# Kernel tuning notes

Measured on AMD Instinct MI355X. Metric: run time of the kernel, lower is better.

The kernel has to match this reference:

```python
import jax, jax.numpy as jnp
import numpy as np

B, T, F = 128, 64, 2048
N, H, C = 1024, 1024, 22  # neurons, hidden_size, num_classes


def setup_inputs() -> dict:
    key = jax.random.key(0)
    ks = jax.random.split(key, 9)
    def w(k, shape, fan_in):
        return jax.random.normal(k, shape, dtype=jnp.float32) / np.sqrt(fan_in)
    return {
        "x": jax.random.normal(ks[0], (B, T, F), dtype=jnp.float32),
        "W1": w(ks[1], (N, F), F),
        "b1": jnp.zeros((N,), jnp.float32),
        "W_ih": w(ks[2], (4 * H, N), N),
        "b_ih": jnp.zeros((4 * H,), jnp.float32),
        "W_hh": w(ks[3], (4 * H, H), H),
        "b_hh": jnp.zeros((4 * H,), jnp.float32),
        "Wc": w(ks[4], (C, H), H),
        "bc": jnp.zeros((C,), jnp.float32),
    }


def reference(x, W1, b1, W_ih, b_ih, W_hh, b_hh, Wc, bc):
    b, t, _ = x.shape
    h0 = jnp.zeros((b, H), x.dtype)
    c0 = jnp.zeros((b, H), x.dtype)
    # Precompute the input-side projections for every step (batched GEMMs):
    z = jax.nn.relu(jnp.einsum("btf,nf->btn", x, W1) + b1)        # [B,T,N]
    xg = jnp.einsum("btn,gn->btg", z, W_ih) + b_ih                 # [B,T,4H]

    def step(carry, xg_t):
        h, c = carry
        gates = xg_t + h @ W_hh.T + b_hh                           # [B,4H]
        i, f, g, o = jnp.split(gates, 4, axis=-1)                  # torch LSTMCell gate order
        c = jax.nn.sigmoid(f) * c + jax.nn.sigmoid(i) * jnp.tanh(g)
        h = jax.nn.sigmoid(o) * jnp.tanh(c)
        return (h, c), h

    _, hs = jax.lax.scan(step, (h0, c0), jnp.swapaxes(xg, 0, 1))    # hs: [T,B,H]
    scores = jnp.einsum("tbh,ch->tbc", hs, Wc) + bc                # [T,B,C]
    scores = jnp.swapaxes(scores, 0, 1).reshape(-1, Wc.shape[0])    # [B*T, C]
    return scores
```

## Files before the change

### kernel.cpp

```cpp
#include <hip/hip_runtime.h>
#include <hip/hip_bf16.h>

typedef short bf16x8 __attribute__((ext_vector_type(8)));
typedef float f32x4 __attribute__((ext_vector_type(4)));

#define B_ 128
#define T_ 64
#define F_ 2048
#define N_ 1024
#define H_ 1024
#define C_ 22

__device__ __forceinline__ ushort f2bf(float f) {
    union { float f; unsigned u; } v; v.f = f;
    unsigned u = v.u;
    unsigned r = (u + 0x7FFFu + ((u >> 16) & 1u)) >> 16;
    return (ushort)r;
}
__device__ __forceinline__ float bf2f(ushort h) {
    union { unsigned u; float f; } v; v.u = ((unsigned)h) << 16;
    return v.f;
}

__global__ __launch_bounds__(256) void cvt_f32_bf16(const float* __restrict__ in,
                                                    ushort* __restrict__ out, int n4) {
    int i = blockIdx.x * blockDim.x + threadIdx.x;
    if (i < n4) {
        float4 v = ((const float4*)in)[i];
        ushort4 o;
        o.x = f2bf(v.x); o.y = f2bf(v.y); o.z = f2bf(v.z); o.w = f2bf(v.w);
        ((ushort4*)out)[i] = o;
    }
}

__global__ __launch_bounds__(256) void cvt_wc(const float* __restrict__ Wc,
                                              ushort* __restrict__ Wcb) {
    int i = blockIdx.x * 256 + threadIdx.x;
    int row = i >> 10;
    Wcb[i] = (row < C_) ? f2bf(Wc[i]) : (ushort)0;
}

__device__ __forceinline__ void gload16(const void* g, void* l) {
    __builtin_amdgcn_global_load_lds(
        (const __attribute__((address_space(1))) unsigned int*)g,
        (__attribute__((address_space(3))) unsigned int*)l, 16, 0, 0);
}

template<int K, bool RELU>
__global__ __launch_bounds__(256) void gemm_bt(const ushort* __restrict__ A,
                                               const ushort* __restrict__ Bm,
                                               const float* __restrict__ bias1,
                                               const float* __restrict__ bias2,
                                               ushort* __restrict__ C,
                                               int Nt, int Nn) {
    __shared__ ushort sA[128 * 32];
    __shared__ ushort sB[128 * 32];
    const int tid = threadIdx.x;
    const int lane = tid & 63, wv = tid >> 6;
    const int tm = blockIdx.x / Nt, tn = blockIdx.x % Nt;
    const int wm = wv >> 1, wn = wv & 1;

    const ushort* gA = A + (size_t)(tm * 128 + (tid >> 2)) * K + (tid & 3) * 8;
    const ushort* gB = Bm + (size_t)(tn * 128 + (tid >> 2)) * K + (tid & 3) * 8;
    char* lAb = (char*)sA + wv * 1024;
    char* lBb = (char*)sB + wv * 1024;

    f32x4 acc[4][4] = {};

    for (int kt = 0; kt < K / 32; kt++) {
        const ushort* a0 = gA + kt * 32;
        const ushort* b0 = gB + kt * 32;
        gload16(a0, lAb);
        gload16(a0 + 64 * K, lAb + 4096);
        gload16(b0, lBb);
        gload16(b0 + 64 * K, lBb + 4096);
        __syncthreads();

        bf16x8 af[4], bfv[4];
#pragma unroll
        for (int i = 0; i < 4; i++)
            af[i] = *(const bf16x8*)&sA[(wm * 64 + i * 16 + (lane & 15)) * 32 + (lane >> 4) * 8];
#pragma unroll
        for (int j = 0; j < 4; j++)
            bfv[j] = *(const bf16x8*)&sB[(wn * 64 + j * 16 + (lane & 15)) * 32 + (lane >> 4) * 8];
#pragma unroll
        for (int i = 0; i < 4; i++)
#pragma unroll
            for (int j = 0; j < 4; j++)
                acc[i][j] = __builtin_amdgcn_mfma_f32_16x16x32_bf16(af[i], bfv[j], acc[i][j], 0, 0, 0);
        __syncthreads();
    }

#pragma unroll
    for (int j = 0; j < 4; j++) {
        int n = tn * 128 + wn * 64 + j * 16 + (lane & 15);
        float bias = bias1[n] + (bias2 ? bias2[n] : 0.f);
#pragma unroll
        for (int i = 0; i < 4; i++) {
            int mbase = tm * 128 + wm * 64 + i * 16 + (lane >> 4) * 4;
#pragma unroll
            for (int r = 0; r < 4; r++) {
                float v = acc[i][j][r] + bias;
                if (RELU) v = v > 0.f ? v : 0.f;
                C[(size_t)(mbase + r) * Nn + n] = f2bf(v);
            }
        }
    }
}

__global__ __launch_bounds__(256, 1) void lstm_persist(ushort* __restrict__ hs,
                                                       const ushort* __restrict__ xg,
                                                       const ushort* __restrict__ Whh,
                                                       unsigned* __restrict__ flags) {
    const int tid = threadIdx.x;
    const int lane = tid & 63;
    const int wv = tid >> 6;
    const int blk = (int)blockIdx.x;
    const int batch0 = (blk >> 6) * 32;
    const int hid0 = (blk & 63) * 16;
    const int gb = blk & ~63;

    bf16x8 breg[32];
    {
        const ushort* br = Whh + (size_t)(wv * H_ + hid0 + (lane & 15)) * H_ + ((lane >> 4) * 8);
#pragma unroll
        for (int ks = 0; ks < 32; ks++) breg[ks] = *(const bf16x8*)(br + ks * 32);
#pragma unroll
        for (int ks = 0; ks < 32; ks++) asm volatile("" : "+v"(breg[ks]));
    }

    __shared__ float lg[4][32][16];

    const int grow = tid >> 3;
    const int gjp = (tid & 7) * 2;
    float c0 = 0.f, c1 = 0.f;

    const int b = batch0 + grow;
    const int jj = hid0 + gjp;
    const ushort* xrow = xg + ((size_t)(b * T_) << 12) + jj;

    for (int t = 0; t < T_; t++) {
        const ushort* xr = xrow + ((size_t)t << 12);
        uint xi = *(const uint*)(xr);
        uint xf = *(const uint*)(xr + 1024);
        uint xgv = *(const uint*)(xr + 2048);
        uint xo = *(const uint*)(xr + 3072);

        const ushort* ar = hs + (size_t)t * (B_ * H_)
                         + (size_t)(batch0 + (lane & 15)) * H_ + ((lane >> 4) * 8);
        f32x4 acc0 = {}, acc1 = {};
#pragma unroll
        for (int ks = 0; ks < 32; ks++) {
            bf16x8 a0 = *(const bf16x8*)(ar + ks * 32);
            bf16x8 a1 = *(const bf16x8*)(ar + 16 * H_ + ks * 32);
            acc0 = __builtin_amdgcn_mfma_f32_16x16x32_bf16(a0, breg[ks], acc0, 0, 0, 0);
            acc1 = __builtin_amdgcn_mfma_f32_16x16x32_bf16(a1, breg[ks], acc1, 0, 0, 0);
        }
#pragma unroll
        for (int r = 0; r < 4; r++) {
            lg[wv][(lane >> 4) * 4 + r][lane & 15] = acc0[r];
            lg[wv][16 + (lane >> 4) * 4 + r][lane & 15] = acc1[r];
        }
        __syncthreads();

        {
            float pi0 = bf2f((ushort)(xi & 0xffff)) + lg[0][grow][gjp];
            float pi1 = bf2f((ushort)(xi >> 16)) + lg[0][grow][gjp + 1];
            float pf0 = bf2f((ushort)(xf & 0xffff)) + lg[1][grow][gjp];
            float pf1 = bf2f((ushort)(xf >> 16)) + lg[1][grow][gjp + 1];
            float pg0 = bf2f((ushort)(xgv & 0xffff)) + lg[2][grow][gjp];
            float pg1 = bf2f((ushort)(xgv >> 16)) + lg[2][grow][gjp + 1];
            float po0 = bf2f((ushort)(xo & 0xffff)) + lg[3][grow][gjp];
            float po1 = bf2f((ushort)(xo >> 16)) + lg[3][grow][gjp + 1];
            float si0 = 1.f / (1.f + expf(-pi0)), si1 = 1.f / (1.f + expf(-pi1));
            float sf0 = 1.f / (1.f + expf(-pf0)), sf1 = 1.f / (1.f + expf(-pf1));
            float tg0 = tanhf(pg0), tg1 = tanhf(pg1);
            float so0 = 1.f / (1.f + expf(-po0)), so1 = 1.f / (1.f + expf(-po1));
            c0 = sf0 * c0 + si0 * tg0;
            c1 = sf1 * c1 + si1 * tg1;
            uint hp = (uint)f2bf(so0 * tanhf(c0)) | ((uint)f2bf(so1 * tanhf(c1)) << 16);
            unsigned* hp32 = (unsigned*)(hs + (size_t)(t + 1) * (B_ * H_) + (size_t)b * H_ + jj);
            __hip_atomic_store(hp32, hp, __ATOMIC_RELAXED, __HIP_MEMORY_SCOPE_AGENT);
        }
        __syncthreads();

        if (t < T_ - 1) {
            if (tid == 0)
                __hip_atomic_store(&flags[blk * 16], (unsigned)(t + 1),
                                   __ATOMIC_RELAXED, __HIP_MEMORY_SCOPE_AGENT);
            if (wv == 0) {
                asm volatile("s_waitcnt vmcnt(0)" ::: "memory");
                for (;;) {
                    unsigned f = __hip_atomic_load(&flags[(gb + lane) * 16],
                                                   __ATOMIC_RELAXED, __HIP_MEMORY_SCOPE_AGENT);
                    if (__ballot(f < (unsigned)(t + 1)) == 0ull) break;
                    __builtin_amdgcn_s_sleep(1);
                }
            }
            __syncthreads();
        }
    }
}

__global__ __launch_bounds__(256) void scores_mfma(const ushort* __restrict__ hs,
                                                   const ushort* __restrict__ Wcb,
                                                   const float* __restrict__ bc,
                                                   float* __restrict__ out) {
    const int tid = threadIdx.x, lane = tid & 63, w = tid >> 6;
    const int r0 = blockIdx.x * 64 + w * 16;
    const int rr = r0 + (lane & 15);
    const int b = rr >> 6, t = rr & 63;
    const ushort* arow = hs + (size_t)(t + 1) * (B_ * H_) + (size_t)b * H_ + ((lane >> 4) * 8);
    const ushort* brow0 = Wcb + (size_t)(lane & 15) * H_ + ((lane >> 4) * 8);
    const ushort* brow1 = brow0 + 16 * H_;

    f32x4 acc0 = {}, acc1 = {};
#pragma unroll
    for (int ks = 0; ks < 32; ks++) {
        bf16x8 a  = *(const bf16x8*)(arow + ks * 32);
        bf16x8 p0 = *(const bf16x8*)(brow0 + ks * 32);
        bf16x8 p1 = *(const bf16x8*)(brow1 + ks * 32);
        acc0 = __builtin_amdgcn_mfma_f32_16x16x32_bf16(a, p0, acc0, 0, 0, 0);
        acc1 = __builtin_amdgcn_mfma_f32_16x16x32_bf16(a, p1, acc1, 0, 0, 0);
    }
#pragma unroll
    for (int nf = 0; nf < 2; nf++) {
        int c = nf * 16 + (lane & 15);
        if (c < C_) {
            float bias = bc[c];
            f32x4 acc = nf ? acc1 : acc0;
#pragma unroll
            for (int r = 0; r < 4; r++) {
                int row = r0 + (lane >> 4) * 4 + r;
                out[(size_t)row * C_ + c] = acc[r] + bias;
            }
        }
    }
}

extern "C" void kernel_launch(void* const* d_in, const int* in_sizes, int n_in,
                              void* d_out, int out_size, void* d_ws, size_t ws_size,
                              hipStream_t stream) {
    const float* x = (const float*)d_in[0];
    const float* W1 = (const float*)d_in[1];
    const float* b1 = (const float*)d_in[2];
    const float* W_ih = (const float*)d_in[3];
    const float* b_ih = (const float*)d_in[4];
    const float* W_hh = (const float*)d_in[5];
    const float* b_hh = (const float*)d_in[6];
    const float* Wc = (const float*)d_in[7];
    const float* bc = (const float*)d_in[8];
    float* out = (float*)d_out;

    char* ws = (char*)d_ws;
    ushort* Xb   = (ushort*)(ws);
    ushort* W1b  = (ushort*)(ws + 33554432);
    ushort* Wihb = (ushort*)(ws + 37748736);
    ushort* Whhb = (ushort*)(ws + 46137344);
    ushort* z    = (ushort*)(ws + 54525952);
    ushort* xg   = (ushort*)(ws + 71303168);
    ushort* hs   = (ushort*)(ws + 138412032);
    ushort* Wcb  = (ushort*)(ws + 155451392);
    unsigned* flags = (unsigned*)(ws + 155516928);

    hipMemsetAsync(hs, 0, (size_t)B_ * H_ * sizeof(ushort), stream);
    hipMemsetAsync(flags, 0, 16384, stream);

    cvt_f32_bf16<<<16384, 256, 0, stream>>>(x, Xb, 4194304);
    cvt_f32_bf16<<<2048, 256, 0, stream>>>(W1, W1b, 524288);
    cvt_f32_bf16<<<4096, 256, 0, stream>>>(W_ih, Wihb, 1048576);
    cvt_f32_bf16<<<4096, 256, 0, stream>>>(W_hh, Whhb, 1048576);
    cvt_wc<<<128, 256, 0, stream>>>(Wc, Wcb);

    gemm_bt<2048, true><<<512, 256, 0, stream>>>(Xb, W1b, b1, nullptr, z, 8, 1024);
    gemm_bt<1024, false><<<2048, 256, 0, stream>>>(z, Wihb, b_ih, b_hh, xg, 32, 4096);

    lstm_persist<<<256, 256, 0, stream>>>(hs, xg, Whhb, flags);

    scores_mfma<<<128, 256, 0, stream>>>(hs, Wcb, bc, out);
}
```

Measured before the change: 782.4 us.

## Repartition persistent LSTM into 16-batch x 32-hidden tiles with 8 waves

```diff
diff --git a/kernel.cpp b/kernel.cpp
--- a/kernel.cpp
+++ b/kernel.cpp
@@ -108,79 +108,75 @@
     }
 }
 
-__global__ __launch_bounds__(256, 1) void lstm_persist(ushort* __restrict__ hs,
+__global__ __launch_bounds__(512, 2) void lstm_persist(ushort* __restrict__ hs,
                                                        const ushort* __restrict__ xg,
                                                        const ushort* __restrict__ Whh,
                                                        unsigned* __restrict__ flags) {
     const int tid = threadIdx.x;
     const int lane = tid & 63;
     const int wv = tid >> 6;
+    const int g = wv >> 1;
+    const int ch = wv & 1;
     const int blk = (int)blockIdx.x;
-    const int batch0 = (blk >> 6) * 32;
-    const int hid0 = (blk & 63) * 16;
-    const int gb = blk & ~63;
+    const int bt = blk & 7;
+    const int hb = blk >> 3;
+    const int batch0 = bt * 16;
+    const int hid0 = hb * 32;
 
     bf16x8 breg[32];
     {
-        const ushort* br = Whh + (size_t)(wv * H_ + hid0 + (lane & 15)) * H_ + ((lane >> 4) * 8);
+        const ushort* br = Whh + (size_t)(g * H_ + hid0 + ch * 16 + (lane & 15)) * H_
+                         + ((lane >> 4) * 8);
 #pragma unroll
         for (int ks = 0; ks < 32; ks++) breg[ks] = *(const bf16x8*)(br + ks * 32);
 #pragma unroll
         for (int ks = 0; ks < 32; ks++) asm volatile("" : "+v"(breg[ks]));
     }
 
-    __shared__ float lg[4][32][16];
-
-    const int grow = tid >> 3;
-    const int gjp = (tid & 7) * 2;
-    float c0 = 0.f, c1 = 0.f;
-
+    __shared__ float lg[4][16][32];
+
+    const int grow = tid >> 5;
+    const int gcol = tid & 31;
     const int b = batch0 + grow;
-    const int jj = hid0 + gjp;
+    const int jj = hid0 + gcol;
     const ushort* xrow = xg + ((size_t)(b * T_) << 12) + jj;
+    float c0 = 0.f;
 
     for (int t = 0; t < T_; t++) {
         const ushort* xr = xrow + ((size_t)t << 12);
-        uint xi = *(const uint*)(xr);
-        uint xf = *(const uint*)(xr + 1024);
-        uint xgv = *(const uint*)(xr + 2048);
-        uint xo = *(const uint*)(xr + 3072);
+        ushort xi = xr[0], xf = xr[1024], xgv = xr[2048], xo = xr[3072];
 
         const ushort* ar = hs + (size_t)t * (B_ * H_)
                          + (size_t)(batch0 + (lane & 15)) * H_ + ((lane >> 4) * 8);
-        f32x4 acc0 = {}, acc1 = {};
+        f32x4 acc = {};
 #pragma unroll
         for (int ks = 0; ks < 32; ks++) {
             bf16x8 a0 = *(const bf16x8*)(ar + ks * 32);
-            bf16x8 a1 = *(const bf16x8*)(ar + 16 * H_ + ks * 32);
-            acc0 = __builtin_amdgcn_mfma_f32_16x16x32_bf16(a0, breg[ks], acc0, 0, 0, 0);
-            acc1 = __builtin_amdgcn_mfma_f32_16x16x32_bf16(a1, breg[ks], acc1, 0, 0, 0);
-        }
-#pragma unroll
-        for (int r = 0; r < 4; r++) {
-            lg[wv][(lane >> 4) * 4 + r][lane & 15] = acc0[r];
-            lg[wv][16 + (lane >> 4) * 4 + r][lane & 15] = acc1[r];
-        }
+            acc = __builtin_amdgcn_mfma_f32_16x16x32_bf16(a0, breg[ks], acc, 0, 0, 0);
+        }
+#pragma unroll
+        for (int r = 0; r < 4; r++)
+            lg[g][(lane >> 4) * 4 + r][ch * 16 + (lane & 15)] = acc[r];
         __syncthreads();
 
         {
-            float pi0 = bf2f((ushort)(xi & 0xffff)) + lg[0][grow][gjp];
-            float pi1 = bf2f((ushort)(xi >> 16)) + lg[0][grow][gjp + 1];
-            float pf0 = bf2f((ushort)(xf & 0xffff)) + lg[1][grow][gjp];
-            float pf1 = bf2f((ushort)(xf >> 16)) + lg[1][grow][gjp + 1];
-            float pg0 = bf2f((ushort)(xgv & 0xffff)) + lg[2][grow][gjp];
-            float pg1 = bf2f((ushort)(xgv >> 16)) + lg[2][grow][gjp + 1];
-            float po0 = bf2f((ushort)(xo & 0xffff)) + lg[3][grow][gjp];
-            float po1 = bf2f((ushort)(xo >> 16)) + lg[3][grow][gjp + 1];
-            float si0 = 1.f / (1.f + expf(-pi0)), si1 = 1.f / (1.f + expf(-pi1));
-            float sf0 = 1.f / (1.f + expf(-pf0)), sf1 = 1.f / (1.f + expf(-pf1));
-            float tg0 = tanhf(pg0), tg1 = tanhf(pg1);
-            float so0 = 1.f / (1.f + expf(-po0)), so1 = 1.f / (1.f + expf(-po1));
-            c0 = sf0 * c0 + si0 * tg0;
-            c1 = sf1 * c1 + si1 * tg1;
-            uint hp = (uint)f2bf(so0 * tanhf(c0)) | ((uint)f2bf(so1 * tanhf(c1)) << 16);
-            unsigned* hp32 = (unsigned*)(hs + (size_t)(t + 1) * (B_ * H_) + (size_t)b * H_ + jj);
-            __hip_atomic_store(hp32, hp, __ATOMIC_RELAXED, __HIP_MEMORY_SCOPE_AGENT);
+            float pi = bf2f(xi)  + lg[0][grow][gcol];
+            float pf = bf2f(xf)  + lg[1][grow][gcol];
+            float pg = bf2f(xgv) + lg[2][grow][gcol];
+            float po = bf2f(xo)  + lg[3][grow][gcol];
+            float si = 1.f / (1.f + expf(-pi));
+            float sf = 1.f / (1.f + expf(-pf));
+            float tg = tanhf(pg);
+            float so = 1.f / (1.f + expf(-po));
+            c0 = sf * c0 + si * tg;
+            ushort hbf = f2bf(so * tanhf(c0));
+            uint other = __shfl_xor((uint)hbf, 1);
+            if ((lane & 1) == 0) {
+                uint hp = (uint)hbf | (other << 16);
+                unsigned* hp32 = (unsigned*)(hs + (size_t)(t + 1) * (B_ * H_)
+                                             + (size_t)b * H_ + jj);
+                __hip_atomic_store(hp32, hp, __ATOMIC_RELAXED, __HIP_MEMORY_SCOPE_AGENT);
+            }
         }
         __syncthreads();
 
@@ -191,7 +187,7 @@
             if (wv == 0) {
                 asm volatile("s_waitcnt vmcnt(0)" ::: "memory");
                 for (;;) {
-                    unsigned f = __hip_atomic_load(&flags[(gb + lane) * 16],
+                    unsigned f = __hip_atomic_load(&flags[((lane & 31) * 8 + bt) * 16],
                                                    __ATOMIC_RELAXED, __HIP_MEMORY_SCOPE_AGENT);
                     if (__ballot(f < (unsigned)(t + 1)) == 0ull) break;
                     __builtin_amdgcn_s_sleep(1);
@@ -275,7 +271,7 @@
     gemm_bt<2048, true><<<512, 256, 0, stream>>>(Xb, W1b, b1, nullptr, z, 8, 1024);
     gemm_bt<1024, false><<<2048, 256, 0, stream>>>(z, Wihb, b_ih, b_hh, xg, 32, 4096);
 
-    lstm_persist<<<256, 256, 0, stream>>>(hs, xg, Whhb, flags);
+    lstm_persist<<<256, 512, 0, stream>>>(hs, xg, Whhb, flags);
 
     scores_mfma<<<128, 256, 0, stream>>>(hs, Wcb, bc, out);
 }
```

After: 820.6 us. 1.05x slower.
